# Optimization experiments

Hardware: AMD Instinct MI355X
Metric: run time of the kernel (lower is better)

The kernel has to match this reference:

```python
import jax, jax.numpy as jnp
import numpy as np

N = 8192
F_IN = 128
F_OUT = 128


def setup_inputs() -> dict:
    key = jax.random.key(0)
    k1, k2, k3, k4, k5 = jax.random.split(key, 5)
    x = jax.random.normal(k1, (N, F_IN), dtype=jnp.float32)
    adj = jax.random.uniform(k2, (N, N), dtype=jnp.float32)
    kernel = jax.random.normal(k3, (F_IN, F_OUT), dtype=jnp.float32) * 0.05
    bias = jax.random.normal(k4, (F_OUT,), dtype=jnp.float32) * 0.05
    beta = jax.random.uniform(k5, (N,), dtype=jnp.float32)
    return {"x": x, "adj": adj, "kernel": kernel, "bias": bias, "beta": beta}


def reference(x, adj, kernel, bias, beta):
    # torch: diag(1/(adj.sum(1)+beta)) @ (adj + diag(beta)) @ x @ kernel + bias
    # (adj + diag(beta)) @ x  ==  adj @ x + beta[:, None] * x  (no NxN temp)
    inv_deg = 1.0 / (jnp.sum(adj, axis=1) + beta)        # [N]
    agg = adj @ x + beta[:, None] * x                     # [N, F_in]
    out = (inv_deg[:, None] * agg) @ kernel + bias        # [N, F_out]
    return out
```

## Files before the change

kernel.cpp:

```cpp
#include <hip/hip_runtime.h>

#define NN 8192
#define FD 128
#define BM 64
#define BK 64
#define LDS_ROW 72

typedef float f32x4 __attribute__((ext_vector_type(4)));
typedef short short8 __attribute__((ext_vector_type(8)));
typedef unsigned short ushort4v __attribute__((ext_vector_type(4)));
typedef unsigned short ushort8v __attribute__((ext_vector_type(8)));

__device__ __forceinline__ unsigned short f2bf(float f) {
  unsigned int u = __builtin_bit_cast(unsigned int, f);
  u += 0x7fffu + ((u >> 16) & 1u);
  return (unsigned short)(u >> 16);
}
__device__ __forceinline__ float bf2f(unsigned short h) {
  unsigned int u = ((unsigned int)h) << 16;
  return __builtin_bit_cast(float, u);
}

__global__ __launch_bounds__(256) void xk_kernel(
    const float* __restrict__ x, const float* __restrict__ kern,
    unsigned short* __restrict__ bfrag, unsigned short* __restrict__ xk_rm) {
  __shared__ __align__(16) unsigned short kl[FD * FD];
  __shared__ __align__(16) float xl[16 * FD];
  const int t = threadIdx.x;
  const int row0 = blockIdx.x * 16;

  #pragma unroll
  for (int j = 0; j < 16; ++j) {
    int idx = (j * 256 + t) * 4;
    f32x4 kv = *(const f32x4*)&kern[idx];
    ushort4v kw;
    #pragma unroll
    for (int q = 0; q < 4; ++q) kw[q] = f2bf(kv[q]);
    *(ushort4v*)&kl[idx] = kw;
  }
  #pragma unroll
  for (int j = 0; j < 2; ++j) {
    int idx = (j * 256 + t) * 4;
    *(f32x4*)&xl[idx] = *(const f32x4*)&x[(size_t)row0 * FD + idx];
  }
  __syncthreads();

  const int r0 = (t >> 5) * 2;
  const int c0 = (t & 31) * 4;
  float acc[2][4] = {};
  #pragma unroll 4
  for (int k = 0; k < FD; ++k) {
    ushort4v kq = *(const ushort4v*)&kl[k * FD + c0];
    float kv[4];
    #pragma unroll
    for (int q = 0; q < 4; ++q) kv[q] = bf2f(kq[q]);
    float x0 = xl[r0 * FD + k];
    float x1 = xl[(r0 + 1) * FD + k];
    #pragma unroll
    for (int q = 0; q < 4; ++q) {
      acc[0][q] += x0 * kv[q];
      acc[1][q] += x1 * kv[q];
    }
  }
  #pragma unroll
  for (int i = 0; i < 2; ++i) {
    const int r = row0 + r0 + i;
    const int kt = r >> 5;
    const int lhi = ((r >> 3) & 3) * 16;
    const int j = r & 7;
    ushort4v ow;
    #pragma unroll
    for (int q = 0; q < 4; ++q) {
      const int c = c0 + q;
      unsigned short bv = f2bf(acc[i][q]);
      ow[q] = bv;
      bfrag[(((size_t)kt * 8 + (c >> 4)) * 64 + (lhi + (c & 15))) * 8 + j] = bv;
    }
    *(ushort4v*)&xk_rm[(size_t)r * FD + c0] = ow;
  }
}

template <int S>
__global__ __launch_bounds__(256, 4) void gcn_mm(
    const float* __restrict__ adj, const unsigned short* __restrict__ bfrag,
    float* __restrict__ parts, float* __restrict__ rowpart) {
  constexpr int KW = NN / S;
  constexpr int NS = KW / BK;
  __shared__ __align__(16) unsigned short sA[2][BM * LDS_ROW];

  const int t = threadIdx.x;
  const int b = blockIdx.x;
  const int s = b & (S - 1);
  const int g = b / S;
  const int row0 = g * BM;
  const int l = t & 63;
  const int w = t >> 6;

  const int su = l >> 4;
  const int sc = l & 15;
  const float* ap = adj + (size_t)(row0 + w * 16 + su) * NN + (size_t)s * KW + sc * 4;
  const int lw = (w * 16 + su) * LDS_ROW + sc * 4;

  const unsigned short* bp = bfrag + (size_t)l * 8;

  f32x4 Lr[4];
  float rs[4] = {0.f, 0.f, 0.f, 0.f};
  f32x4 acc[4][2] = {};

  #pragma unroll
  for (int i = 0; i < 4; ++i)
    Lr[i] = *(const f32x4*)(ap + (size_t)i * 4 * NN);
  #pragma unroll
  for (int i = 0; i < 4; ++i) {
    ushort4v cw;
    #pragma unroll
    for (int q = 0; q < 4; ++q) cw[q] = f2bf(Lr[i][q]);
    rs[i] += Lr[i][0] + Lr[i][1] + Lr[i][2] + Lr[i][3];
    *(ushort4v*)&sA[0][lw + i * 4 * LDS_ROW] = cw;
  }
  __syncthreads();

  #pragma unroll 2
  for (int st = 0; st < NS; ++st) {
    const int cur = st & 1;
    if (st + 1 < NS) {
      #pragma unroll
      for (int i = 0; i < 4; ++i)
        Lr[i] = *(const f32x4*)(ap + (size_t)i * 4 * NN + (st + 1) * BK);
    }
    const int ktg = s * (KW / 32) + st * 2;
    ushort8v bF[2][2];
    #pragma unroll
    for (int h = 0; h < 2; ++h)
      #pragma unroll
      for (int ci = 0; ci < 2; ++ci)
        bF[h][ci] = *(const ushort8v*)(bp + (((size_t)(ktg + h) * 8 + (w * 2 + ci)) * 64) * 8);
    #pragma unroll
    for (int h = 0; h < 2; ++h) {
      #pragma unroll
      for (int rb = 0; rb < 4; ++rb) {
        const int row = rb * 16 + (l & 15);
        short8 aF = *(const short8*)&sA[cur][row * LDS_ROW + h * 32 + (l >> 4) * 8];
        acc[rb][0] = __builtin_amdgcn_mfma_f32_16x16x32_bf16(aF, bF[h][0], acc[rb][0], 0, 0, 0);
        acc[rb][1] = __builtin_amdgcn_mfma_f32_16x16x32_bf16(aF, bF[h][1], acc[rb][1], 0, 0, 0);
      }
    }
    if (st + 1 < NS) {
      #pragma unroll
      for (int i = 0; i < 4; ++i) {
        ushort4v cw;
        #pragma unroll
        for (int q = 0; q < 4; ++q) cw[q] = f2bf(Lr[i][q]);
        rs[i] += Lr[i][0] + Lr[i][1] + Lr[i][2] + Lr[i][3];
        *(ushort4v*)&sA[cur ^ 1][lw + i * 4 * LDS_ROW] = cw;
      }
    }
    __syncthreads();
  }

  #pragma unroll
  for (int i = 0; i < 4; ++i) {
    rs[i] += __shfl_xor(rs[i], 1);
    rs[i] += __shfl_xor(rs[i], 2);
    rs[i] += __shfl_xor(rs[i], 4);
    rs[i] += __shfl_xor(rs[i], 8);
  }
  if (sc == 0) {
    #pragma unroll
    for (int i = 0; i < 4; ++i)
      rowpart[(size_t)s * NN + row0 + w * 16 + i * 4 + su] = rs[i];
  }

  float* pp = parts + ((size_t)s * NN + row0) * FD + w * 32;
  #pragma unroll
  for (int rb = 0; rb < 4; ++rb)
    #pragma unroll
    for (int ci = 0; ci < 2; ++ci)
      #pragma unroll
      for (int j = 0; j < 4; ++j) {
        const int r = rb * 16 + ((l >> 4) << 2) + j;
        pp[(size_t)r * FD + ci * 16 + (l & 15)] = acc[rb][ci][j];
      }
}

__global__ __launch_bounds__(256) void gcn_fin(
    const float* __restrict__ parts, const float* __restrict__ rowpart,
    const unsigned short* __restrict__ xk_rm, const float* __restrict__ beta,
    const float* __restrict__ bias, float* __restrict__ out, int S) {
  const int t = threadIdx.x;
  const int r = blockIdx.x * 16 + (t >> 4);
  const int c0 = (t & 15) * 8;

  float rsum = 0.f;
  for (int s = 0; s < S; ++s) rsum += rowpart[(size_t)s * NN + r];
  const float bt = beta[r];
  const float inv = 1.0f / (rsum + bt);

  f32x4 acc0 = {0.f, 0.f, 0.f, 0.f};
  f32x4 acc1 = {0.f, 0.f, 0.f, 0.f};
  for (int s = 0; s < S; ++s) {
    const float* p = parts + ((size_t)s * NN + r) * FD + c0;
    acc0 += *(const f32x4*)p;
    acc1 += *(const f32x4*)(p + 4);
  }
  ushort8v xv = *(const ushort8v*)&xk_rm[(size_t)r * FD + c0];
  f32x4 o0, o1;
  #pragma unroll
  for (int q = 0; q < 4; ++q) {
    o0[q] = (acc0[q] + bt * bf2f(xv[q])) * inv + bias[c0 + q];
    o1[q] = (acc1[q] + bt * bf2f(xv[4 + q])) * inv + bias[c0 + 4 + q];
  }
  *(f32x4*)&out[(size_t)r * FD + c0] = o0;
  *(f32x4*)&out[(size_t)r * FD + c0 + 4] = o1;
}

extern "C" void kernel_launch(void* const* d_in, const int* in_sizes, int n_in,
                              void* d_out, int out_size, void* d_ws, size_t ws_size,
                              hipStream_t stream) {
  const float* x    = (const float*)d_in[0];
  const float* adj  = (const float*)d_in[1];
  const float* kern = (const float*)d_in[2];
  const float* bias = (const float*)d_in[3];
  const float* beta = (const float*)d_in[4];
  float* out = (float*)d_out;

  char* ws = (char*)d_ws;
  unsigned short* bfrag = (unsigned short*)ws;
  unsigned short* xk_rm = (unsigned short*)(ws + (size_t)NN * FD * 2);
  const size_t off_rowpart = (size_t)NN * FD * 4;
  float* rowpart = (float*)(ws + off_rowpart);
  const size_t off_parts = off_rowpart + (size_t)8 * NN * 4;
  float* parts = (float*)(ws + off_parts);

  int S = 8;
  while (S > 1 && off_parts + (size_t)S * NN * FD * 4 > ws_size) S >>= 1;

  hipLaunchKernelGGL(xk_kernel, dim3(NN / 16), dim3(256), 0, stream,
                     x, kern, bfrag, xk_rm);

  dim3 blk(256);
  switch (S) {
    case 8: hipLaunchKernelGGL(gcn_mm<8>, dim3(128 * 8), blk, 0, stream, adj, bfrag, parts, rowpart); break;
    case 4: hipLaunchKernelGGL(gcn_mm<4>, dim3(128 * 4), blk, 0, stream, adj, bfrag, parts, rowpart); break;
    case 2: hipLaunchKernelGGL(gcn_mm<2>, dim3(128 * 2), blk, 0, stream, adj, bfrag, parts, rowpart); break;
    default: hipLaunchKernelGGL(gcn_mm<1>, dim3(128), blk, 0, stream, adj, bfrag, parts, rowpart); break;
  }

  hipLaunchKernelGGL(gcn_fin, dim3(NN / 16), dim3(256), 0, stream,
                     parts, rowpart, xk_rm, beta, bias, out, S);
}
```

Measured before the change: 98.85 us.

## Give each wave private 32-row adj tiles, drop block syncs, store bf16 partials

```diff
diff --git a/kernel.cpp b/kernel.cpp
--- a/kernel.cpp
+++ b/kernel.cpp
@@ -2,9 +2,8 @@
 
 #define NN 8192
 #define FD 128
-#define BM 64
 #define BK 64
-#define LDS_ROW 72
+#define LDSR 72
 
 typedef float f32x4 __attribute__((ext_vector_type(4)));
 typedef short short8 __attribute__((ext_vector_type(8)));
@@ -81,110 +80,103 @@
 }
 
 template <int S>
-__global__ __launch_bounds__(256, 4) void gcn_mm(
+__global__ __launch_bounds__(256) void gcn_mm(
     const float* __restrict__ adj, const unsigned short* __restrict__ bfrag,
-    float* __restrict__ parts, float* __restrict__ rowpart) {
+    unsigned short* __restrict__ parts, float* __restrict__ rowpart) {
   constexpr int KW = NN / S;
   constexpr int NS = KW / BK;
-  __shared__ __align__(16) unsigned short sA[2][BM * LDS_ROW];
+  __shared__ __align__(16) unsigned short sA[4][2][32 * LDSR];
 
   const int t = threadIdx.x;
+  const int l = t & 63;
+  const int w = t >> 6;
   const int b = blockIdx.x;
   const int s = b & (S - 1);
-  const int g = b / S;
-  const int row0 = g * BM;
-  const int l = t & 63;
-  const int w = t >> 6;
-
-  const int su = l >> 4;
-  const int sc = l & 15;
-  const float* ap = adj + (size_t)(row0 + w * 16 + su) * NN + (size_t)s * KW + sc * 4;
-  const int lw = (w * 16 + su) * LDS_ROW + sc * 4;
-
+  const int row0 = (b / S) * 128 + w * 32;
+  const int kbase = s * KW;
+
+  const float* ap = adj + (size_t)(row0 + (l >> 4)) * NN + kbase + (l & 15) * 4;
+  unsigned short* sw = &sA[w][0][0];
+  const int wofs = (l >> 4) * LDSR + (l & 15) * 4;
   const unsigned short* bp = bfrag + (size_t)l * 8;
 
-  f32x4 Lr[4];
-  float rs[4] = {0.f, 0.f, 0.f, 0.f};
-  f32x4 acc[4][2] = {};
-
-  #pragma unroll
-  for (int i = 0; i < 4; ++i)
+  f32x4 Lr[8];
+  f32x4 acc[2][8] = {};
+  float rs[8] = {0.f, 0.f, 0.f, 0.f, 0.f, 0.f, 0.f, 0.f};
+
+  #pragma unroll
+  for (int i = 0; i < 8; ++i)
     Lr[i] = *(const f32x4*)(ap + (size_t)i * 4 * NN);
   #pragma unroll
-  for (int i = 0; i < 4; ++i) {
+  for (int i = 0; i < 8; ++i) {
     ushort4v cw;
     #pragma unroll
     for (int q = 0; q < 4; ++q) cw[q] = f2bf(Lr[i][q]);
     rs[i] += Lr[i][0] + Lr[i][1] + Lr[i][2] + Lr[i][3];
-    *(ushort4v*)&sA[0][lw + i * 4 * LDS_ROW] = cw;
-  }
-  __syncthreads();
+    *(ushort4v*)&sw[wofs + i * 4 * LDSR] = cw;
+  }
 
   #pragma unroll 2
   for (int st = 0; st < NS; ++st) {
     const int cur = st & 1;
     if (st + 1 < NS) {
       #pragma unroll
-      for (int i = 0; i < 4; ++i)
+      for (int i = 0; i < 8; ++i)
         Lr[i] = *(const f32x4*)(ap + (size_t)i * 4 * NN + (st + 1) * BK);
     }
     const int ktg = s * (KW / 32) + st * 2;
-    ushort8v bF[2][2];
-    #pragma unroll
-    for (int h = 0; h < 2; ++h)
-      #pragma unroll
-      for (int ci = 0; ci < 2; ++ci)
-        bF[h][ci] = *(const ushort8v*)(bp + (((size_t)(ktg + h) * 8 + (w * 2 + ci)) * 64) * 8);
     #pragma unroll
     for (int h = 0; h < 2; ++h) {
-      #pragma unroll
-      for (int rb = 0; rb < 4; ++rb) {
-        const int row = rb * 16 + (l & 15);
-        short8 aF = *(const short8*)&sA[cur][row * LDS_ROW + h * 32 + (l >> 4) * 8];
-        acc[rb][0] = __builtin_amdgcn_mfma_f32_16x16x32_bf16(aF, bF[h][0], acc[rb][0], 0, 0, 0);
-        acc[rb][1] = __builtin_amdgcn_mfma_f32_16x16x32_bf16(aF, bF[h][1], acc[rb][1], 0, 0, 0);
+      const int abase = cur * 32 * LDSR + h * 32 + (l >> 4) * 8;
+      short8 aF0 = *(const short8*)&sw[abase + (l & 15) * LDSR];
+      short8 aF1 = *(const short8*)&sw[abase + (16 + (l & 15)) * LDSR];
+      #pragma unroll
+      for (int cb = 0; cb < 8; ++cb) {
+        ushort8v Bf = *(const ushort8v*)(bp + (((size_t)(ktg + h) * 8 + cb) << 9));
+        acc[0][cb] = __builtin_amdgcn_mfma_f32_16x16x32_bf16(aF0, Bf, acc[0][cb], 0, 0, 0);
+        acc[1][cb] = __builtin_amdgcn_mfma_f32_16x16x32_bf16(aF1, Bf, acc[1][cb], 0, 0, 0);
       }
     }
     if (st + 1 < NS) {
-      #pragma unroll
-      for (int i = 0; i < 4; ++i) {
+      const int nb = (cur ^ 1) * 32 * LDSR;
+      #pragma unroll
+      for (int i = 0; i < 8; ++i) {
         ushort4v cw;
         #pragma unroll
         for (int q = 0; q < 4; ++q) cw[q] = f2bf(Lr[i][q]);
         rs[i] += Lr[i][0] + Lr[i][1] + Lr[i][2] + Lr[i][3];
-        *(ushort4v*)&sA[cur ^ 1][lw + i * 4 * LDS_ROW] = cw;
+        *(ushort4v*)&sw[nb + wofs + i * 4 * LDSR] = cw;
       }
     }
-    __syncthreads();
-  }
-
-  #pragma unroll
-  for (int i = 0; i < 4; ++i) {
+  }
+
+  #pragma unroll
+  for (int i = 0; i < 8; ++i) {
     rs[i] += __shfl_xor(rs[i], 1);
     rs[i] += __shfl_xor(rs[i], 2);
     rs[i] += __shfl_xor(rs[i], 4);
     rs[i] += __shfl_xor(rs[i], 8);
   }
-  if (sc == 0) {
-    #pragma unroll
-    for (int i = 0; i < 4; ++i)
-      rowpart[(size_t)s * NN + row0 + w * 16 + i * 4 + su] = rs[i];
-  }
-
-  float* pp = parts + ((size_t)s * NN + row0) * FD + w * 32;
-  #pragma unroll
-  for (int rb = 0; rb < 4; ++rb)
-    #pragma unroll
-    for (int ci = 0; ci < 2; ++ci)
+  if ((l & 15) == 0) {
+    #pragma unroll
+    for (int i = 0; i < 8; ++i)
+      rowpart[(size_t)s * NN + row0 + i * 4 + (l >> 4)] = rs[i];
+  }
+
+  unsigned short* pp = parts + ((size_t)s * NN + row0) * FD;
+  #pragma unroll
+  for (int rf = 0; rf < 2; ++rf)
+    #pragma unroll
+    for (int cb = 0; cb < 8; ++cb)
       #pragma unroll
       for (int j = 0; j < 4; ++j) {
-        const int r = rb * 16 + ((l >> 4) << 2) + j;
-        pp[(size_t)r * FD + ci * 16 + (l & 15)] = acc[rb][ci][j];
+        const int r = rf * 16 + ((l >> 4) << 2) + j;
+        pp[(size_t)r * FD + cb * 16 + (l & 15)] = f2bf(acc[rf][cb][j]);
       }
 }
 
 __global__ __launch_bounds__(256) void gcn_fin(
-    const float* __restrict__ parts, const float* __restrict__ rowpart,
+    const unsigned short* __restrict__ parts, const float* __restrict__ rowpart,
     const unsigned short* __restrict__ xk_rm, const float* __restrict__ beta,
     const float* __restrict__ bias, float* __restrict__ out, int S) {
   const int t = threadIdx.x;
@@ -196,19 +188,18 @@
   const float bt = beta[r];
   const float inv = 1.0f / (rsum + bt);
 
-  f32x4 acc0 = {0.f, 0.f, 0.f, 0.f};
-  f32x4 acc1 = {0.f, 0.f, 0.f, 0.f};
+  float a[8] = {0.f, 0.f, 0.f, 0.f, 0.f, 0.f, 0.f, 0.f};
   for (int s = 0; s < S; ++s) {
-    const float* p = parts + ((size_t)s * NN + r) * FD + c0;
-    acc0 += *(const f32x4*)p;
-    acc1 += *(const f32x4*)(p + 4);
+    ushort8v pv = *(const ushort8v*)&parts[((size_t)s * NN + r) * FD + c0];
+    #pragma unroll
+    for (int q = 0; q < 8; ++q) a[q] += bf2f(pv[q]);
   }
   ushort8v xv = *(const ushort8v*)&xk_rm[(size_t)r * FD + c0];
   f32x4 o0, o1;
   #pragma unroll
   for (int q = 0; q < 4; ++q) {
-    o0[q] = (acc0[q] + bt * bf2f(xv[q])) * inv + bias[c0 + q];
-    o1[q] = (acc1[q] + bt * bf2f(xv[4 + q])) * inv + bias[c0 + 4 + q];
+    o0[q] = (a[q] + bt * bf2f(xv[q])) * inv + bias[c0 + q];
+    o1[q] = (a[4 + q] + bt * bf2f(xv[4 + q])) * inv + bias[c0 + 4 + q];
   }
   *(f32x4*)&out[(size_t)r * FD + c0] = o0;
   *(f32x4*)&out[(size_t)r * FD + c0 + 4] = o1;
@@ -230,20 +221,20 @@
   const size_t off_rowpart = (size_t)NN * FD * 4;
   float* rowpart = (float*)(ws + off_rowpart);
   const size_t off_parts = off_rowpart + (size_t)8 * NN * 4;
-  float* parts = (float*)(ws + off_parts);
+  unsigned short* parts = (unsigned short*)(ws + off_parts);
 
   int S = 8;
-  while (S > 1 && off_parts + (size_t)S * NN * FD * 4 > ws_size) S >>= 1;
+  while (S > 1 && off_parts + (size_t)S * NN * FD * 2 > ws_size) S >>= 1;
 
   hipLaunchKernelGGL(xk_kernel, dim3(NN / 16), dim3(256), 0, stream,
                      x, kern, bfrag, xk_rm);
 
   dim3 blk(256);
   switch (S) {
-    case 8: hipLaunchKernelGGL(gcn_mm<8>, dim3(128 * 8), blk, 0, stream, adj, bfrag, parts, rowpart); break;
-    case 4: hipLaunchKernelGGL(gcn_mm<4>, dim3(128 * 4), blk, 0, stream, adj, bfrag, parts, rowpart); break;
-    case 2: hipLaunchKernelGGL(gcn_mm<2>, dim3(128 * 2), blk, 0, stream, adj, bfrag, parts, rowpart); break;
-    default: hipLaunchKernelGGL(gcn_mm<1>, dim3(128), blk, 0, stream, adj, bfrag, parts, rowpart); break;
+    case 8: hipLaunchKernelGGL(gcn_mm<8>, dim3(64 * 8), blk, 0, stream, adj, bfrag, parts, rowpart); break;
+    case 4: hipLaunchKernelGGL(gcn_mm<4>, dim3(64 * 4), blk, 0, stream, adj, bfrag, parts, rowpart); break;
+    case 2: hipLaunchKernelGGL(gcn_mm<2>, dim3(64 * 2), blk, 0, stream, adj, bfrag, parts, rowpart); break;
+    default: hipLaunchKernelGGL(gcn_mm<1>, dim3(64), blk, 0, stream, adj, bfrag, parts, rowpart); break;
   }
 
   hipLaunchKernelGGL(gcn_fin, dim3(NN / 16), dim3(256), 0, stream,
```

Measured after the change: 85.15 us. 13.9% less time.
